# Kernel optimization log

Measured on AMD Instinct MI355X. Metric: run time of the kernel, lower is better.

## Reference

```python
import jax, jax.numpy as jnp
import numpy as np


def pool_mat(size, out):
    # PyTorch AdaptiveAvgPool2d binning: start=floor(i*size/out), end=ceil((i+1)*size/out)
    M = np.zeros((out, size), dtype=np.float32)
    for i in range(out):
        s = (i * size) // out
        e = -((-(i + 1) * size) // out)
        M[i, s:e] = 1.0 / (e - s)
    return jnp.asarray(M)


def setup_inputs() -> dict:
    key = jax.random.key(0)
    ks = jax.random.split(key, 14)
    B, C, H, R = 4096, 256, 7, 1024
    D = C * H * H  # 12544
    def nrm(k, shape, scale):
        return jax.random.normal(k, shape, dtype=jnp.float32) * scale
    return {
        "x": nrm(ks[0], (B, C, H, H), 1.0),
        "w1": nrm(ks[1], (C, C), 1.0 / np.sqrt(C)),
        "w2": nrm(ks[2], (C, C), 1.0 / np.sqrt(C)),
        "w3": nrm(ks[3], (C, C), 1.0 / np.sqrt(C)),
        "w6": nrm(ks[4], (C, C), 1.0 / np.sqrt(C)),
        "w_cat": nrm(ks[5], (C, 4 * C), 1.0 / np.sqrt(4 * C)),
        "fc6c_w": nrm(ks[6], (R, D), 1.0 / np.sqrt(D)),
        "fc6c_b": nrm(ks[7], (R,), 0.01),
        "fc7c_w": nrm(ks[8], (R, R), 1.0 / np.sqrt(R)),
        "fc7c_b": nrm(ks[9], (R,), 0.01),
        "fc6r_w": nrm(ks[10], (R, D), 1.0 / np.sqrt(D)),
        "fc6r_b": nrm(ks[11], (R,), 0.01),
        "fc7r_w": nrm(ks[12], (R, R), 1.0 / np.sqrt(R)),
        "fc7r_b": nrm(ks[13], (R,), 0.01),
    }


def _scale_branch(x, M, w_conv):
    # x: [B,C,H,W]; M: [P1d,H] adaptive-pool matrix; w_conv: [C,C] 1x1 conv weight
    B, C, H, W = x.shape
    pooled = jnp.einsum('ph,bchw,qw->bcpq', M, x, M).reshape(B, C, -1)  # [B,C,P]
    xt = x.reshape(B, C, H * W).transpose(0, 2, 1)                     # [B,HW,C]
    attn = jax.nn.softmax(jnp.einsum('bnc,bcp->bnp', xt, pooled), axis=-1)
    out = jnp.einsum('bcp,bnp->bcn', pooled, attn).reshape(B, C, H, W)
    return jax.nn.relu(jnp.einsum('oc,bchw->bohw', w_conv, out))


def reference(x, w1, w2, w3, w6, w_cat, fc6c_w, fc6c_b, fc7c_w, fc7c_b,
              fc6r_w, fc6r_b, fc7r_w, fc7r_b):
    B, C, H, W = x.shape
    s1 = _scale_branch(x, pool_mat(H, 1), w1)
    s2 = _scale_branch(x, pool_mat(H, 2), w2)
    s3 = _scale_branch(x, pool_mat(H, 3), w3)
    s6 = _scale_branch(x, pool_mat(H, 6), w6)
    cat = jnp.concatenate([s1, s2, s3, s6], axis=1)                    # [B,4C,H,W]
    xf = x + jnp.einsum('oc,bchw->bohw', w_cat, cat)                   # fusing 1x1 conv + residual
    f = xf.reshape(B, -1)                                              # [B, C*H*W]
    xc = jax.nn.relu(f @ fc6c_w.T + fc6c_b)
    xc = xc @ fc7c_w.T + fc7c_b
    xr = jax.nn.relu(f @ fc6r_w.T + fc6r_b)
    xr = jax.nn.relu(xr @ fc7r_w.T + fc7r_b)
    return xc, xr
```

## Files before the change

### kernel.cpp

```cpp
#include <hip/hip_runtime.h>

typedef unsigned short u16;
typedef unsigned int   u32;
typedef float  f4v    __attribute__((ext_vector_type(4)));
typedef short  short8 __attribute__((ext_vector_type(8)));
typedef __bf16 bf16x8 __attribute__((ext_vector_type(8)));


__device__ __forceinline__ u16 f2bf(float f) {
  union { float f; u32 u; } v; v.f = f;
  return (u16)((v.u + 0x7FFFu + ((v.u >> 16) & 1u)) >> 16);
}
__device__ __forceinline__ float bf2f(u16 h) {
  union { u32 u; float f; } v; v.u = (u32)h << 16;
  return v.f;
}

__device__ __forceinline__ int seg_gb(int k) { return (k == 0) ? 0 : (k == 1) ? 4096 : (k == 2) ? 20480 : 57344; }
__device__ __forceinline__ int seg_pc(int k) { return (k == 0) ? 1 : (k == 1) ? 4 : (k == 2) ? 9 : 36; }
__device__ __forceinline__ int seg_s0(int k) { return (k == 0) ? 0 : (k == 1) ? 1 : (k == 2) ? 5 : 14; }

__device__ __forceinline__ void gl16(const void* g, void* l) {
  __builtin_amdgcn_global_load_lds(
      (const __attribute__((address_space(1))) unsigned int*)g,
      (__attribute__((address_space(3))) unsigned int*)l, 16, 0, 0);
}

__global__ __launch_bounds__(256) void k_pack(
    const float* __restrict__ w1, const float* __restrict__ w2,
    const float* __restrict__ w3, const float* __restrict__ w6,
    const float* __restrict__ wcat,
    const float* __restrict__ f6c, const float* __restrict__ f6r,
    const float* __restrict__ f7c, const float* __restrict__ f7r,
    const float* __restrict__ b6c, const float* __restrict__ b6r,
    u16* __restrict__ W14B, u16* __restrict__ WCATB, u16* __restrict__ W6P,
    u16* __restrict__ W7B, float* __restrict__ BIAS6)
{
  const u32 total = 28313600u;
  for (u32 t = blockIdx.x * 256u + threadIdx.x; t < total; t += gridDim.x * 256u) {
    if (t < 262144u) {
      u32 a = t >> 16, i = t & 65535u;
      const float* s = (a == 0) ? w1 : (a == 1) ? w2 : (a == 2) ? w3 : w6;
      W14B[t] = f2bf(s[i]);
    } else if (t < 524288u) {
      u32 i = t - 262144u;
      WCATB[i] = f2bf(wcat[i]);
    } else if (t < 26214400u) {
      u32 j = t - 524288u;
      u32 r = j / 12544u, rem = j - r * 12544u;
      u32 n = rem >> 8, c = rem & 255u;
      const float* s = (r < 1024u) ? f6c : f6r;
      W6P[j] = f2bf(s[(size_t)(r & 1023u) * 12544u + c * 49u + n]);
    } else if (t < 28311552u) {
      u32 j = t - 26214400u;
      W7B[j] = f2bf((j < 1048576u) ? f7c[j] : f7r[j - 1048576u]);
    } else {
      u32 j = t - 28311552u;
      BIAS6[j] = (j < 1024u) ? b6c[j] : b6r[j - 1024u];
    }
  }
}

#define PST 272
#define SST 52

__device__ __forceinline__ void pool_geom(int p, int& k, int& pl, int& r0, int& nr, int& c0, int& nc) {
  if (p == 0)      { k = 0; pl = 0;      r0 = 0; nr = 7; c0 = 0; nc = 7; }
  else if (p < 5)  { k = 1; pl = p - 1;  int i = pl >> 1, j = pl & 1; r0 = i * 3; nr = 4; c0 = j * 3; nc = 4; }
  else if (p < 14) { k = 2; pl = p - 5;  int i = pl / 3,  j = pl % 3; r0 = i * 2; nr = 3; c0 = j * 2; nc = 3; }
  else             { k = 3; pl = p - 14; int i = pl / 6,  j = pl % 6; r0 = i;     nr = 2; c0 = j;     nc = 2; }
}

__global__ __launch_bounds__(1024) void k_pool_attn(
    const float* __restrict__ x, u16* __restrict__ POOL, float* __restrict__ ATTN)
{
  __shared__ __align__(16) u16 Xh[49 * PST];
  __shared__ __align__(16) u16 Xl[49 * PST];
  __shared__ __align__(16) u16 Ph[50 * PST];
  __shared__ __align__(16) u16 Pl[50 * PST];
  __shared__ float Ss[49 * SST];
  const int b = blockIdx.x;
  const int t = threadIdx.x;
  const float* xb = x + (size_t)b * 12544;

  for (int j = t; j < 12544; j += 1024) {
    int c = j / 49, n = j - c * 49;
    float v = xb[j];
    u16 hi = f2bf(v);
    u16 lo = f2bf(v - bf2f(hi));
    Xh[n * PST + c] = hi;
    Xl[n * PST + c] = lo;
  }
  __syncthreads();

  for (int j = t; j < 12800; j += 1024) {
    int p = j >> 8, c = j & 255;
    int k, pl, r0, nr, c0, nc;
    pool_geom(p, k, pl, r0, nr, c0, nc);
    float s = 0.f;
    for (int r = 0; r < nr; ++r)
      for (int q = 0; q < nc; ++q) {
        int idx = ((r0 + r) * 7 + c0 + q) * PST + c;
        s += bf2f(Xh[idx]) + bf2f(Xl[idx]);
      }
    s *= (1.0f / (float)(nr * nc));
    u16 hi = f2bf(s);
    u16 lo = f2bf(s - bf2f(hi));
    Ph[p * PST + c] = hi;
    Pl[p * PST + c] = lo;
    POOL[((size_t)(seg_gb(k) + b * seg_pc(k) + pl)) * 256 + c] = hi;
  }
  __syncthreads();

  {
    const int wv = t >> 6, l = t & 63;
    const int lr = l & 15, lg = l >> 4;
    const int mi = wv & 3, pi = wv >> 2;
    int an = mi * 16 + lr; if (an > 48) an = 48;
    int bp = pi * 16 + lr; if (bp > 49) bp = 49;
    f4v acc = {};
    #pragma unroll
    for (int kk = 0; kk < 8; ++kk) {
      int ko = kk * 32 + lg * 8;
      short8 ah = *(const short8*)(Xh + an * PST + ko);
      short8 al = *(const short8*)(Xl + an * PST + ko);
      short8 bh = *(const short8*)(Ph + bp * PST + ko);
      short8 bl = *(const short8*)(Pl + bp * PST + ko);
      acc = __builtin_amdgcn_mfma_f32_16x16x32_bf16(
          __builtin_bit_cast(bf16x8, ah), __builtin_bit_cast(bf16x8, bh), acc, 0, 0, 0);
      acc = __builtin_amdgcn_mfma_f32_16x16x32_bf16(
          __builtin_bit_cast(bf16x8, ah), __builtin_bit_cast(bf16x8, bl), acc, 0, 0, 0);
      acc = __builtin_amdgcn_mfma_f32_16x16x32_bf16(
          __builtin_bit_cast(bf16x8, al), __builtin_bit_cast(bf16x8, bh), acc, 0, 0, 0);
    }
    #pragma unroll
    for (int r = 0; r < 4; ++r) {
      int n = mi * 16 + lg * 4 + r;
      int p = pi * 16 + lr;
      if (n < 49 && p < 50) Ss[n * SST + p] = acc[r];
    }
  }
  __syncthreads();

  if (t < 196) {
    int n = t >> 2, k = t & 3;
    int s0 = seg_s0(k), pc = seg_pc(k);
    float m = -3.0e38f;
    for (int i = 0; i < pc; ++i) m = fmaxf(m, Ss[n * SST + s0 + i]);
    float sum = 0.f;
    for (int i = 0; i < pc; ++i) sum += __expf(Ss[n * SST + s0 + i] - m);
    float inv = 1.0f / sum;
    float* ab = ATTN + (size_t)b * 2450 + n * 50 + s0;
    for (int i = 0; i < pc; ++i) ab[i] = __expf(Ss[n * SST + s0 + i] - m) * inv;
  }
}

__global__ __launch_bounds__(512, 4) void k_scat_conv(
    const u16* __restrict__ Y, const float* __restrict__ ATTN,
    const u16* __restrict__ WCATB, const float* __restrict__ x,
    u16* __restrict__ XF)
{
  __shared__ __align__(16) u16 attnB[49 * 52];
  __shared__ __align__(16) u16 xS[49 * 264];
  __shared__ __align__(16) u16 YT[256 * 64];
  __shared__ __align__(16) u16 scatCh[64 * 128];
  const int b = blockIdx.x;
  const int t = threadIdx.x;
  const int wv = t >> 6, l = t & 63;
  const int lr = l & 15, lg = l >> 4;

  for (int i = t; i < 2450; i += 512) {
    int n = i / 50, p = i - n * 50;
    attnB[n * 52 + p] = f2bf(ATTN[(size_t)b * 2450 + i]);
  }
  for (int i = t; i < 12544; i += 512) {
    int c = i / 49, n = i - c * 49;
    xS[n * 264 + c] = f2bf(x[(size_t)b * 12544 + i]);
  }
  {
    int4 zz; zz.x = 0; zz.y = 0; zz.z = 0; zz.w = 0;
    int4* z = (int4*)YT;
    #pragma unroll
    for (int i = 0; i < 4; ++i) z[t + i * 512] = zz;
  }
  __syncthreads();

  f4v acc[4][2] = {};

  for (int k = 0; k < 4; ++k) {
    const int pc = seg_pc(k), s0 = seg_s0(k), gb = seg_gb(k);
    const int kks = (k == 3) ? 2 : 1;

    for (int i = t; i < pc * 256; i += 512) {
      int p = i >> 8, c = i & 255;
      u32 sig = (u32)(((c & 7) ^ ((c >> 3) & 7)) << 4);
      u16 v = Y[((size_t)(gb + b * pc + p)) * 256 + c];
      *(u16*)((char*)YT + c * 128 + ((2u * p) ^ sig)) = v;
    }
    __syncthreads();

    for (int h = 0; h < 2; ++h) {
      {
        const int cB = h * 128 + wv * 16 + lr;
        const u32 sig = (u32)(((cB & 7) ^ ((cB >> 3) & 7)) << 4);
        f4v sacc[4] = {};
        for (int kk = 0; kk < kks; ++kk) {
          short8 bfv = *(const short8*)((const char*)YT + cB * 128 + (((u32)(kk * 64 + lg * 16)) ^ sig));
          #pragma unroll
          for (int mi = 0; mi < 4; ++mi) {
            int n = mi * 16 + lr;
            short8 af;
            #pragma unroll
            for (int j = 0; j < 8; ++j) {
              int p = kk * 32 + lg * 8 + j;
              u16 v = attnB[(n < 49 ? n : 0) * 52 + s0 + (p < pc ? p : 0)];
              af[j] = (n < 49 && p < pc) ? (short)v : (short)0;
            }
            sacc[mi] = __builtin_amdgcn_mfma_f32_16x16x32_bf16(
                __builtin_bit_cast(bf16x8, af), __builtin_bit_cast(bf16x8, bfv),
                sacc[mi], 0, 0, 0);
          }
        }
        #pragma unroll
        for (int mi = 0; mi < 4; ++mi) {
          #pragma unroll
          for (int r = 0; r < 4; ++r) {
            int n = mi * 16 + lg * 4 + r;
            int op = wv * 16 + lr;
            *(u16*)((char*)scatCh + n * 256 + ((2u * op) ^ (u32)((n & 7) << 4))) =
                f2bf(fmaxf(sacc[mi][r], 0.f));
          }
        }
      }
      __syncthreads();
      {
        #pragma unroll
        for (int kk = 0; kk < 4; ++kk) {
          short8 af2[4];
          #pragma unroll
          for (int mi = 0; mi < 4; ++mi) {
            int n = mi * 16 + lr;
            af2[mi] = *(const short8*)((const char*)scatCh + n * 256 +
                        (((u32)(kk * 64 + lg * 16)) ^ (u32)((n & 7) << 4)));
          }
          #pragma unroll
          for (int ni = 0; ni < 2; ++ni) {
            int c = wv * 32 + ni * 16 + lr;
            short8 bf2 = *(const short8*)(WCATB + (size_t)c * 1024 +
                          k * 256 + h * 128 + kk * 32 + lg * 8);
            #pragma unroll
            for (int mi = 0; mi < 4; ++mi)
              acc[mi][ni] = __builtin_amdgcn_mfma_f32_16x16x32_bf16(
                  __builtin_bit_cast(bf16x8, af2[mi]), __builtin_bit_cast(bf16x8, bf2),
                  acc[mi][ni], 0, 0, 0);
          }
        }
      }
      __syncthreads();
    }
  }

  #pragma unroll
  for (int mi = 0; mi < 4; ++mi) {
    #pragma unroll
    for (int r = 0; r < 4; ++r) {
      int n = mi * 16 + lg * 4 + r;
      if (n < 49) {
        #pragma unroll
        for (int ni = 0; ni < 2; ++ni) {
          int c = wv * 32 + ni * 16 + lr;
          union { u32 u; float f; } xv; xv.u = (u32)xS[n * 264 + c] << 16;
          XF[((size_t)b * 49 + n) * 256 + c] = f2bf(acc[mi][ni][r] + xv.f);
        }
      }
    }
  }
}

template<bool OBF16>
__global__ __launch_bounds__(256) void gemm_k(
    const u16* __restrict__ A, int lda,
    const u16* __restrict__ W, int ldb,
    void* __restrict__ Cout, int ldc,
    int mtiles, int ntiles, int scW, int kchunk,
    const float* __restrict__ bias, int relu)
{
  __shared__ char lds[32768];
  char* ldsA = lds;
  char* ldsB = lds + 16384;
  const int tid = threadIdx.x;
  const int wv = tid >> 6, l = tid & 63;

  const int nwg = gridDim.x;
  const int q = nwg >> 3, r8 = nwg & 7;
  const int xcd = blockIdx.x & 7, pos = blockIdx.x >> 3;
  int wg = (xcd < r8 ? xcd * (q + 1) : r8 * (q + 1) + (xcd - r8) * q) + pos;

  const int sub = mtiles * ntiles;
  const int ks = wg / sub; wg -= ks * sub;
  const int band = mtiles * scW;
  const int sc = wg / band; wg -= sc * band;
  const int mt = wg / scW;
  const int nt = sc * scW + (wg - mt * scW);
  const int m0 = mt * 128, n0 = nt * 128;
  const int k0 = ks * kchunk;

  const char* Ab = (const char*)(A + (size_t)m0 * lda + k0);
  const char* Bb = (const char*)(W + (size_t)n0 * ldb + k0);
  const int ldab = lda * 2, ldbb = ldb * 2;
  const int rloc = l >> 3;
  const int swz = ((l & 7) ^ rloc) << 4;

  auto stage = [&](int kt) {
    const char* Ak = Ab + kt * 2 + swz;
    const char* Bk = Bb + kt * 2 + swz;
    #pragma unroll
    for (int it = 0; it < 4; ++it) {
      int rb = (it * 4 + wv) * 8;
      gl16(Ak + (size_t)(rb + rloc) * ldab, ldsA + rb * 128);
      gl16(Bk + (size_t)(rb + rloc) * ldbb, ldsB + rb * 128);
    }
  };

  const int wr = (wv >> 1) * 64, wc = (wv & 1) * 64;
  const int lr = l & 15, lg = l >> 4;
  f4v acc[4][4] = {};

  stage(0);
  for (int kt = 0; kt < kchunk; kt += 64) {
    __syncthreads();
    #pragma unroll
    for (int kk = 0; kk < 2; ++kk) {
      short8 af[4], bfv[4];
      #pragma unroll
      for (int mi = 0; mi < 4; ++mi) {
        int rA = wr + mi * 16 + lr;
        af[mi] = *(const short8*)(ldsA + rA * 128 + ((kk * 64 + lg * 16) ^ ((rA & 7) << 4)));
      }
      #pragma unroll
      for (int ni = 0; ni < 4; ++ni) {
        int rB = wc + ni * 16 + lr;
        bfv[ni] = *(const short8*)(ldsB + rB * 128 + ((kk * 64 + lg * 16) ^ ((rB & 7) << 4)));
      }
      #pragma unroll
      for (int mi = 0; mi < 4; ++mi)
        #pragma unroll
        for (int ni = 0; ni < 4; ++ni)
          acc[mi][ni] = __builtin_amdgcn_mfma_f32_16x16x32_bf16(
              __builtin_bit_cast(bf16x8, af[mi]),
              __builtin_bit_cast(bf16x8, bfv[ni]),
              acc[mi][ni], 0, 0, 0);
    }
    if (kt + 64 < kchunk) { __syncthreads(); stage(kt + 64); }
  }

  const size_t crow0 = (size_t)ks * mtiles * 128 + m0;
  #pragma unroll
  for (int ni = 0; ni < 4; ++ni) {
    int gc = n0 + wc + ni * 16 + lr;
    float bv = bias ? bias[gc] : 0.f;
    #pragma unroll
    for (int mi = 0; mi < 4; ++mi) {
      #pragma unroll
      for (int j = 0; j < 4; ++j) {
        size_t gr = crow0 + wr + mi * 16 + lg * 4 + j;
        float v = acc[mi][ni][j] + bv;
        if (relu) v = fmaxf(v, 0.f);
        if (OBF16) ((u16*)Cout)[gr * ldc + gc] = f2bf(v);
        else       ((float*)Cout)[gr * ldc + gc] = v;
      }
    }
  }
}

__global__ __launch_bounds__(256) void k_red6(
    const float* __restrict__ P, const float* __restrict__ bias, u16* __restrict__ XC1)
{
  const size_t base = ((size_t)blockIdx.x * 256 + threadIdx.x) * 8;
  f4v a0 = *(const f4v*)(P + base);
  f4v a1 = *(const f4v*)(P + base + 4);
  const float* P2 = P + 8388608;
  f4v b0 = *(const f4v*)(P2 + base);
  f4v b1 = *(const f4v*)(P2 + base + 4);
  int col = (int)(base & 2047u);
  u16 o[8];
  #pragma unroll
  for (int j = 0; j < 4; ++j) o[j]     = f2bf(fmaxf(a0[j] + b0[j] + bias[col + j], 0.f));
  #pragma unroll
  for (int j = 0; j < 4; ++j) o[4 + j] = f2bf(fmaxf(a1[j] + b1[j] + bias[col + 4 + j], 0.f));
  *(int4*)(XC1 + base) = *(const int4*)(&o[0]);
}

extern "C" void kernel_launch(void* const* d_in, const int* in_sizes, int n_in,
                              void* d_out, int out_size, void* d_ws, size_t ws_size,
                              hipStream_t stream)
{
  (void)in_sizes; (void)n_in; (void)out_size; (void)ws_size;
  const float* x    = (const float*)d_in[0];
  const float* w1   = (const float*)d_in[1];
  const float* w2   = (const float*)d_in[2];
  const float* w3   = (const float*)d_in[3];
  const float* w6   = (const float*)d_in[4];
  const float* wcat = (const float*)d_in[5];
  const float* f6cw = (const float*)d_in[6];
  const float* f6cb = (const float*)d_in[7];
  const float* f7cw = (const float*)d_in[8];
  const float* f7cb = (const float*)d_in[9];
  const float* f6rw = (const float*)d_in[10];
  const float* f6rb = (const float*)d_in[11];
  const float* f7rw = (const float*)d_in[12];
  const float* f7rb = (const float*)d_in[13];

  char* ws = (char*)d_ws;
  u16*   W14B  = (u16*)(ws);
  u16*   WCATB = (u16*)(ws + 524288);
  u16*   W6P   = (u16*)(ws + 1048576);
  u16*   W7B   = (u16*)(ws + 52428800);
  float* BIAS6 = (float*)(ws + 56623104);
  u16*   POOL  = (u16*)(ws + 56631296);
  u16*   XF    = POOL;
  float* ATTN  = (float*)(ws + 161488896);
  u16*   XC1   = (u16*)(ws + 161488896);
  u16*   Y     = (u16*)(ws + 201629696);
  float* PART  = (float*)(ws + 201629696);

  k_pack<<<dim3(2048), dim3(256), 0, stream>>>(w1, w2, w3, w6, wcat, f6cw, f6rw,
                                               f7cw, f7rw, f6cb, f6rb,
                                               W14B, WCATB, W6P, W7B, BIAS6);
  k_pool_attn<<<dim3(4096), dim3(1024), 0, stream>>>(x, POOL, ATTN);

  for (int k = 0; k < 4; ++k) {
    int gb = (k == 0) ? 0 : (k == 1) ? 4096 : (k == 2) ? 20480 : 57344;
    int pc = (k == 0) ? 1 : (k == 1) ? 4 : (k == 2) ? 9 : 36;
    int mtl = 32 * pc;
    gemm_k<true><<<dim3(mtl * 2), dim3(256), 0, stream>>>(
        POOL + (size_t)gb * 256, 256, W14B + k * 65536, 256,
        (void*)(Y + (size_t)gb * 256), 256, mtl, 2, 2, 256, nullptr, 0);
  }

  k_scat_conv<<<dim3(4096), dim3(512), 0, stream>>>(Y, ATTN, WCATB, x, XF);

  gemm_k<false><<<dim3(1024), dim3(256), 0, stream>>>(
      XF, 12544, W6P, 12544, (void*)PART, 2048, 32, 16, 8, 6272, nullptr, 0);
  k_red6<<<dim3(4096), dim3(256), 0, stream>>>(PART, BIAS6, XC1);

  float* out = (float*)d_out;
  gemm_k<false><<<dim3(256), dim3(256), 0, stream>>>(
      XC1, 2048, W7B, 1024, (void*)out, 1024, 32, 8, 8, 1024, f7cb, 0);
  gemm_k<false><<<dim3(256), dim3(256), 0, stream>>>(
      XC1 + 1024, 2048, W7B + 1048576, 1024,
      (void*)(out + (size_t)4096 * 1024), 1024, 32, 8, 8, 1024, f7rb, 1);
}
```

Baseline: 1.776 ms.

## Restructure scatter-conv LDS layout: pre-split attention, vectorized stores, staged output

Reorganizes the k_scat_conv shared memory into a single union buffer. Attention is pre-laid out per segment so MFMA operands load as 16-byte vectors instead of per-element gathers with bounds checks, and the MFMA operand roles are swapped so scatter results are written as 4-wide vectors. The residual x load moves to the epilogue, reusing freed LDS, and output is staged in LDS for coalesced 16-byte global stores. The unswizzled YT layout with 72-element stride and the extra barriers may add bank conflicts or synchronization cost.

```diff
diff --git a/kernel.cpp b/kernel.cpp
--- a/kernel.cpp
+++ b/kernel.cpp
@@ -2,9 +2,10 @@
 
 typedef unsigned short u16;
 typedef unsigned int   u32;
-typedef float  f4v    __attribute__((ext_vector_type(4)));
-typedef short  short8 __attribute__((ext_vector_type(8)));
-typedef __bf16 bf16x8 __attribute__((ext_vector_type(8)));
+typedef float  f4v     __attribute__((ext_vector_type(4)));
+typedef short  short4v __attribute__((ext_vector_type(4)));
+typedef short  short8  __attribute__((ext_vector_type(8)));
+typedef __bf16 bf16x8  __attribute__((ext_vector_type(8)));
 
 
 __device__ __forceinline__ u16 f2bf(float f) {
@@ -160,76 +161,64 @@
     const u16* __restrict__ WCATB, const float* __restrict__ x,
     u16* __restrict__ XF)
 {
-  __shared__ __align__(16) u16 attnB[49 * 52];
-  __shared__ __align__(16) u16 xS[49 * 264];
-  __shared__ __align__(16) u16 YT[256 * 64];
-  __shared__ __align__(16) u16 scatCh[64 * 128];
+  __shared__ __align__(16) char U[73728];
   const int b = blockIdx.x;
   const int t = threadIdx.x;
   const int wv = t >> 6, l = t & 63;
   const int lr = l & 15, lg = l >> 4;
 
-  for (int i = t; i < 2450; i += 512) {
-    int n = i / 50, p = i - n * 50;
-    attnB[n * 52 + p] = f2bf(ATTN[(size_t)b * 2450 + i]);
-  }
-  for (int i = t; i < 12544; i += 512) {
-    int c = i / 49, n = i - c * 49;
-    xS[n * 264 + c] = f2bf(x[(size_t)b * 12544 + i]);
-  }
+  u16* YT = (u16*)U;
+  u16* AT = (u16*)(U + 36864);
+  char* SC = U + 57344;
+
   {
     int4 zz; zz.x = 0; zz.y = 0; zz.z = 0; zz.w = 0;
-    int4* z = (int4*)YT;
-    #pragma unroll
-    for (int i = 0; i < 4; ++i) z[t + i * 512] = zz;
-  }
-  __syncthreads();
+    int4* z = (int4*)U;
+    for (int i = t; i < 3584; i += 512) z[i] = zz;
+  }
+  __syncthreads();
+
+  for (int i = t; i < 2450; i += 512) {
+    int n = i / 50, pg = i - n * 50;
+    int k = (pg < 1) ? 0 : (pg < 5) ? 1 : (pg < 14) ? 2 : 3;
+    int pl = pg - seg_s0(k);
+    AT[n * 160 + k * 32 + pl] = f2bf(ATTN[(size_t)b * 2450 + i]);
+  }
 
   f4v acc[4][2] = {};
 
   for (int k = 0; k < 4; ++k) {
-    const int pc = seg_pc(k), s0 = seg_s0(k), gb = seg_gb(k);
+    const int pc = seg_pc(k), gb = seg_gb(k);
     const int kks = (k == 3) ? 2 : 1;
 
     for (int i = t; i < pc * 256; i += 512) {
       int p = i >> 8, c = i & 255;
-      u32 sig = (u32)(((c & 7) ^ ((c >> 3) & 7)) << 4);
-      u16 v = Y[((size_t)(gb + b * pc + p)) * 256 + c];
-      *(u16*)((char*)YT + c * 128 + ((2u * p) ^ sig)) = v;
+      YT[c * 72 + p] = Y[((size_t)(gb + b * pc + p)) * 256 + c];
     }
     __syncthreads();
 
     for (int h = 0; h < 2; ++h) {
       {
-        const int cB = h * 128 + wv * 16 + lr;
-        const u32 sig = (u32)(((cB & 7) ^ ((cB >> 3) & 7)) << 4);
+        const int cy = h * 128 + wv * 16 + lr;
         f4v sacc[4] = {};
         for (int kk = 0; kk < kks; ++kk) {
-          short8 bfv = *(const short8*)((const char*)YT + cB * 128 + (((u32)(kk * 64 + lg * 16)) ^ sig));
+          short8 yf = *(const short8*)(YT + cy * 72 + kk * 32 + lg * 8);
           #pragma unroll
-          for (int mi = 0; mi < 4; ++mi) {
-            int n = mi * 16 + lr;
-            short8 af;
-            #pragma unroll
-            for (int j = 0; j < 8; ++j) {
-              int p = kk * 32 + lg * 8 + j;
-              u16 v = attnB[(n < 49 ? n : 0) * 52 + s0 + (p < pc ? p : 0)];
-              af[j] = (n < 49 && p < pc) ? (short)v : (short)0;
-            }
-            sacc[mi] = __builtin_amdgcn_mfma_f32_16x16x32_bf16(
-                __builtin_bit_cast(bf16x8, af), __builtin_bit_cast(bf16x8, bfv),
-                sacc[mi], 0, 0, 0);
+          for (int ni = 0; ni < 4; ++ni) {
+            short8 af = *(const short8*)(AT + (ni * 16 + lr) * 160 + k * 32 + kk * 32 + lg * 8);
+            sacc[ni] = __builtin_amdgcn_mfma_f32_16x16x32_bf16(
+                __builtin_bit_cast(bf16x8, yf), __builtin_bit_cast(bf16x8, af),
+                sacc[ni], 0, 0, 0);
           }
         }
+        const u32 opb = (u32)((wv * 16 + lg * 4) * 2);
         #pragma unroll
-        for (int mi = 0; mi < 4; ++mi) {
+        for (int ni = 0; ni < 4; ++ni) {
+          int n = ni * 16 + lr;
+          short4v ov;
           #pragma unroll
-          for (int r = 0; r < 4; ++r) {
-            int n = mi * 16 + lg * 4 + r;
-            int op = wv * 16 + lr;
-            *(u16*)((char*)scatCh + n * 256 + ((2u * op) ^ (u32)((n & 7) << 4))) =
-                f2bf(fmaxf(sacc[mi][r], 0.f));
-          }
+          for (int r = 0; r < 4; ++r) ov[r] = (short)f2bf(fmaxf(sacc[ni][r], 0.f));
+          *(short4v*)(SC + n * 256 + (opb ^ (u32)((n & 7) << 4))) = ov;
         }
       }
       __syncthreads();
@@ -240,7 +229,7 @@
           #pragma unroll
           for (int mi = 0; mi < 4; ++mi) {
             int n = mi * 16 + lr;
-            af2[mi] = *(const short8*)((const char*)scatCh + n * 256 +
+            af2[mi] = *(const short8*)(SC + n * 256 +
                         (((u32)(kk * 64 + lg * 16)) ^ (u32)((n & 7) << 4)));
           }
           #pragma unroll
@@ -260,6 +249,13 @@
     }
   }
 
+  u16* xres = (u16*)U;
+  u16* res  = (u16*)(U + 26624);
+  for (int i = t; i < 12544; i += 512) {
+    int c = i / 49, n = i - c * 49;
+    xres[n * 264 + c] = f2bf(x[(size_t)b * 12544 + i]);
+  }
+  __syncthreads();
   #pragma unroll
   for (int mi = 0; mi < 4; ++mi) {
     #pragma unroll
@@ -269,11 +265,15 @@
         #pragma unroll
         for (int ni = 0; ni < 2; ++ni) {
           int c = wv * 32 + ni * 16 + lr;
-          union { u32 u; float f; } xv; xv.u = (u32)xS[n * 264 + c] << 16;
-          XF[((size_t)b * 49 + n) * 256 + c] = f2bf(acc[mi][ni][r] + xv.f);
+          res[n * 264 + c] = f2bf(acc[mi][ni][r] + bf2f(xres[n * 264 + c]));
         }
       }
     }
+  }
+  __syncthreads();
+  for (int j = t; j < 1568; j += 512) {
+    int n = j >> 5, w = j & 31;
+    *(int4*)(XF + ((size_t)b * 49 + n) * 256 + w * 8) = *(const int4*)(res + n * 264 + w * 8);
   }
 }
 
```

After: 1.661 ms. 6.5% less time.
